# Kernel optimization log

Hardware: AMD Instinct MI355X
Metric: run time of the kernel (lower is better)

Reference implementation:

```python
import jax, jax.numpy as jnp
import numpy as np

B, N, H, NH = 2, 2048, 1024, 16
HD = H // NH


def setup_inputs() -> dict:
    key = jax.random.key(0)
    ks = jax.random.split(key, 12)
    s = 0.02
    inp = {
        "q": jax.random.normal(ks[0], (B, N, H), jnp.float32),
        "k": jax.random.normal(ks[1], (B, N, H), jnp.float32),
        "v": jax.random.normal(ks[2], (B, N, H), jnp.float32),
        # causal mask, broadcast over batch and heads
        "mask": jnp.tril(jnp.ones((N, N), jnp.float32))[None, None, :, :],
        "Wq": jax.random.normal(ks[3], (H, H), jnp.float32) * s,
        "bq": jnp.zeros((H,), jnp.float32),
        "Wk": jax.random.normal(ks[4], (H, H), jnp.float32) * s,
        "bk": jnp.zeros((H,), jnp.float32),
        "Wv": jax.random.normal(ks[5], (H, H), jnp.float32) * s,
        "bv": jnp.zeros((H,), jnp.float32),
        "Wp": jax.random.normal(ks[6], (H, H), jnp.float32) * s,
        "bp": jnp.zeros((H,), jnp.float32),
    }
    return inp


def _split_heads(x):
    # [b, n, (h d)] -> [b, h, n, d]
    b, n, _ = x.shape
    return x.reshape(b, n, NH, HD).transpose(0, 2, 1, 3)


def reference(q, k, v, mask, Wq, bq, Wk, bk, Wv, bv, Wp, bp):
    Q = _split_heads(q @ Wq.T + bq)                      # [b,h,n,d]
    K = _split_heads(k @ Wk.T + bk)
    V = _split_heads(v @ Wv.T + bv)
    scores = jnp.einsum("bhnd,bhmd->bhnm", Q, K) / jnp.sqrt(jnp.float32(HD))
    scores = jnp.where(mask == 0, -jnp.inf, scores)
    attn = jax.nn.softmax(scores, axis=-1)
    out = jnp.einsum("bhnm,bhmd->bhnd", attn, V)         # [b,h,n,d]
    out = out.transpose(0, 2, 1, 3).reshape(q.shape[0], q.shape[1], H)
    # dropout is identity in eval mode
    return out @ Wp.T + bp
```

## Files before the change

kernel.cpp:

```cpp
#include <hip/hip_runtime.h>


typedef unsigned short ushortT;
typedef unsigned int uintT;
typedef __attribute__((ext_vector_type(8))) short short8;
typedef __attribute__((ext_vector_type(4))) float f32x4;

#define M_ROWS 4096
#define KDIM   1024
#define NDIM   1024
#define SEQ    2048
#define HDHEAD 64

__device__ __forceinline__ float bf2f(ushortT s) {
    union { unsigned u; float f; } v; v.u = ((unsigned)s) << 16; return v.f;
}
__device__ __forceinline__ ushortT f2bf(float x) {
    union { float f; unsigned u; } v; v.f = x;
    return (ushortT)((v.u + 0x7fffu + ((v.u >> 16) & 1u)) >> 16);
}

__device__ __forceinline__ bool detect_f32(const uintT* w) {
    int hits = 0;
#pragma unroll
    for (int i = 0; i < 16; ++i) {
        const unsigned e = (w[i] >> 7) & 0xffu;
        hits += (e >= 118u && e <= 131u) ? 1 : 0;
    }
    return hits < 8;
}

__device__ __forceinline__ short8 cvt8(const float* p) {
    f32x4 a = *(const f32x4*)p;
    f32x4 b = *(const f32x4*)(p + 4);
    short8 r;
    r[0] = (short)f2bf(a[0]); r[1] = (short)f2bf(a[1]);
    r[2] = (short)f2bf(a[2]); r[3] = (short)f2bf(a[3]);
    r[4] = (short)f2bf(b[0]); r[5] = (short)f2bf(b[1]);
    r[6] = (short)f2bf(b[2]); r[7] = (short)f2bf(b[3]);
    return r;
}

__device__ __forceinline__ void gl2lds16(const ushortT* g, ushortT* l) {
    __builtin_amdgcn_global_load_lds(
        (const __attribute__((address_space(1))) void*)g,
        (__attribute__((address_space(3))) void*)l,
        16, 0, 0);
}

__device__ __forceinline__ void bar_lgkm() {
    __builtin_amdgcn_sched_barrier(0);
    asm volatile("s_waitcnt lgkmcnt(0)" ::: "memory");
    __builtin_amdgcn_s_barrier();
    __builtin_amdgcn_sched_barrier(0);
}

__global__ __launch_bounds__(256) void convert_kernel(
    const void* __restrict__ q, const void* __restrict__ k, const void* __restrict__ v,
    const void* __restrict__ Wq, const void* __restrict__ Wk,
    const void* __restrict__ Wv, const void* __restrict__ Wp,
    const void* __restrict__ bq, const void* __restrict__ bk,
    const void* __restrict__ bv, const void* __restrict__ bp,
    ushortT* __restrict__ dst) {
    const bool f32m = detect_f32((const uintT*)q);
    const size_t u = (size_t)blockIdx.x * 256 + threadIdx.x;

    const void* src; size_t soff, doff;
    if (u < 1572864u) {
        const int seg = (int)(u >> 19);
        const size_t o = u & 524287u;
        src  = seg == 0 ? q : (seg == 1 ? k : v);
        soff = o * 8;
        doff = (size_t)seg * 4194304u + o * 8;
    } else if (u < 2097152u) {
        const size_t u2 = u - 1572864u;
        const int seg = (int)(u2 >> 17);
        const size_t o = u2 & 131071u;
        src  = seg == 0 ? Wq : (seg == 1 ? Wk : (seg == 2 ? Wv : Wp));
        soff = o * 8;
        doff = 12582912u + (size_t)seg * 1048576u + o * 8;
    } else {
        const size_t u3 = u - 2097152u;
        const int seg = (int)(u3 >> 7);
        const size_t o = u3 & 127u;
        src  = seg == 0 ? bq : (seg == 1 ? bk : (seg == 2 ? bv : bp));
        soff = o * 8;
        doff = 16777216u + (size_t)seg * 1024u + o * 8;
    }

    if (f32m)
        *(short8*)(dst + doff) = cvt8((const float*)src + soff);
    else
        *(short8*)(dst + doff) = *(const short8*)((const ushortT*)src + soff);
}

__device__ __forceinline__ void gemm_body(const void* __restrict__ Av,
                                          const void* __restrict__ Wv_,
                                          const void* __restrict__ biasv,
                                          void* __restrict__ Cv,
                                          bool a_f32, bool w_f32, bool c_f32,
                                          float cscale, bool vt_store) {
    __shared__ ushortT ldsA[128 * 64];
    __shared__ ushortT ldsB[128 * 64];

    const int tid  = threadIdx.x;
    const int lane = tid & 63;
    const int wid  = tid >> 6;
    const int bm   = blockIdx.x;
    const int bn   = blockIdx.y;
    const int wm   = wid >> 1;
    const int wn   = wid & 1;

    const int srow = lane >> 2;
    const int scol = (lane & 3) * 8;

    f32x4 acc[4][4];
#pragma unroll
    for (int i = 0; i < 4; ++i)
#pragma unroll
        for (int j = 0; j < 4; ++j) acc[i][j] = (f32x4){0.f, 0.f, 0.f, 0.f};

    const int fr   = lane & 15;
    const int quad = lane >> 4;

    for (int kt = 0; kt < KDIM / 64; ++kt) {
        const int k0 = kt * 64;
        if (!a_f32 && !w_f32) {
#pragma unroll
            for (int t = 0; t < 4; ++t) {
                const int chunk = wid * 4 + t;
                const int kh  = chunk >> 3;
                const int r16 = (chunk & 7) * 16;
                const size_t ra = (size_t)(bm * 128 + r16 + srow) * KDIM + k0 + kh * 32 + scol;
                const size_t rw = (size_t)(bn * 128 + r16 + srow) * KDIM + k0 + kh * 32 + scol;
                gl2lds16((const ushortT*)Av + ra, ldsA + chunk * 512);
                gl2lds16((const ushortT*)Wv_ + rw, ldsB + chunk * 512);
            }
        } else {
            short8 ta[4], tb[4];
#pragma unroll
            for (int t = 0; t < 4; ++t) {
                const int chunk = wid * 4 + t;
                const int kh  = chunk >> 3;
                const int r16 = (chunk & 7) * 16;
                const size_t ra = (size_t)(bm * 128 + r16 + srow) * KDIM + k0 + kh * 32 + scol;
                const size_t rw = (size_t)(bn * 128 + r16 + srow) * KDIM + k0 + kh * 32 + scol;
                ta[t] = a_f32 ? cvt8((const float*)Av + ra)
                              : *(const short8*)((const ushortT*)Av + ra);
                tb[t] = w_f32 ? cvt8((const float*)Wv_ + rw)
                              : *(const short8*)((const ushortT*)Wv_ + rw);
            }
#pragma unroll
            for (int t = 0; t < 4; ++t) {
                const int chunk = wid * 4 + t;
                *(short8*)(ldsA + chunk * 512 + lane * 8) = ta[t];
                *(short8*)(ldsB + chunk * 512 + lane * 8) = tb[t];
            }
        }
        __syncthreads();

#pragma unroll
        for (int s = 0; s < 2; ++s) {
            short8 aF[4], bF[4];
#pragma unroll
            for (int i = 0; i < 4; ++i)
                aF[i] = *(const short8*)(ldsA + s * 4096 + (wm * 64 + i * 16 + fr) * 32 + quad * 8);
#pragma unroll
            for (int j = 0; j < 4; ++j)
                bF[j] = *(const short8*)(ldsB + s * 4096 + (wn * 64 + j * 16 + fr) * 32 + quad * 8);
#pragma unroll
            for (int i = 0; i < 4; ++i)
#pragma unroll
                for (int j = 0; j < 4; ++j)
                    acc[i][j] = __builtin_amdgcn_mfma_f32_16x16x32_bf16(aF[i], bF[j], acc[i][j], 0, 0, 0);
        }
        __syncthreads();
    }

#pragma unroll
    for (int j = 0; j < 4; ++j) {
        const int col = bn * 128 + wn * 64 + j * 16 + fr;
        const float bv = w_f32 ? ((const float*)biasv)[col]
                               : bf2f(((const ushortT*)biasv)[col]);
#pragma unroll
        for (int i = 0; i < 4; ++i) {
            const int row0 = bm * 128 + wm * 64 + i * 16 + quad * 4;
#pragma unroll
            for (int r = 0; r < 4; ++r) {
                const float val = (acc[i][j][r] + bv) * cscale;
                const int row = row0 + r;
                if (vt_store) {
                    const int bb = row >> 11, n = row & 2047;
                    const int hh = col >> 6,  d = col & 63;
                    ((ushortT*)Cv)[(size_t)((bb * 16 + hh) * 64 + d) * SEQ + n] = f2bf(val);
                } else if (c_f32) {
                    ((float*)Cv)[(size_t)row * NDIM + col] = val;
                } else {
                    ((ushortT*)Cv)[(size_t)row * NDIM + col] = f2bf(val);
                }
            }
        }
    }
}

__global__ __launch_bounds__(256, 3) void qkv_proj_kernel(
    const void* __restrict__ q, const void* __restrict__ k, const void* __restrict__ v,
    const void* __restrict__ Wq, const void* __restrict__ Wk, const void* __restrict__ Wv,
    const void* __restrict__ bq, const void* __restrict__ bk, const void* __restrict__ bv,
    ushortT* __restrict__ Qp, ushortT* __restrict__ Kp, ushortT* __restrict__ Vt) {
    const bool f32m = detect_f32((const uintT*)q);
    const void* A; const void* W; const void* bias; ushortT* C;
    float cscale = 1.f; bool vt = false;
    if (blockIdx.z == 0)      { A = q; W = Wq; bias = bq; C = Qp; cscale = 0.125f; }
    else if (blockIdx.z == 1) { A = k; W = Wk; bias = bk; C = Kp; }
    else                      { A = v; W = Wv; bias = bv; C = Vt; vt = true; }
    gemm_body(A, W, bias, (void*)C, f32m, f32m, false, cscale, vt);
}

__global__ __launch_bounds__(256, 2) void out_proj_kernel(
    const ushortT* __restrict__ A, const void* __restrict__ W,
    const void* __restrict__ bias, void* __restrict__ C,
    const void* __restrict__ qdet) {
    const bool wf = detect_f32((const uintT*)W);
    const bool cf = detect_f32((const uintT*)qdet);

    __shared__ ushortT ldsA[128 * 64];
    __shared__ ushortT ldsB[64 * 64];

    const int tid  = threadIdx.x;
    const int lane = tid & 63;
    const int wid  = tid >> 6;
    const int bm   = blockIdx.x;
    const int bn   = blockIdx.y;

    const int srow = lane >> 2;
    const int scol = (lane & 3) * 8;
    const int fr   = lane & 15;
    const int quad = lane >> 4;

    f32x4 acc[2][4];
#pragma unroll
    for (int i = 0; i < 2; ++i)
#pragma unroll
        for (int j = 0; j < 4; ++j) acc[i][j] = (f32x4){0.f, 0.f, 0.f, 0.f};

    for (int kt = 0; kt < KDIM / 64; ++kt) {
        const int k0 = kt * 64;
        if (!wf) {
#pragma unroll
            for (int t = 0; t < 4; ++t) {
                const int chunk = wid * 4 + t;
                const int kh  = chunk >> 3;
                const int r16 = (chunk & 7) * 16;
                const size_t ra = (size_t)(bm * 128 + r16 + srow) * KDIM + k0 + kh * 32 + scol;
                gl2lds16(A + ra, ldsA + chunk * 512);
            }
#pragma unroll
            for (int t = 0; t < 2; ++t) {
                const int chunk = wid * 2 + t;
                const int kh  = chunk >> 2;
                const int r16 = (chunk & 3) * 16;
                const size_t rw = (size_t)(bn * 64 + r16 + srow) * KDIM + k0 + kh * 32 + scol;
                gl2lds16((const ushortT*)W + rw, ldsB + chunk * 512);
            }
        } else {
            short8 ta[4], tb[2];
#pragma unroll
            for (int t = 0; t < 4; ++t) {
                const int chunk = wid * 4 + t;
                const int kh  = chunk >> 3;
                const int r16 = (chunk & 7) * 16;
                const size_t ra = (size_t)(bm * 128 + r16 + srow) * KDIM + k0 + kh * 32 + scol;
                ta[t] = *(const short8*)(A + ra);
            }
#pragma unroll
            for (int t = 0; t < 2; ++t) {
                const int chunk = wid * 2 + t;
                const int kh  = chunk >> 2;
                const int r16 = (chunk & 3) * 16;
                const size_t rw = (size_t)(bn * 64 + r16 + srow) * KDIM + k0 + kh * 32 + scol;
                tb[t] = cvt8((const float*)W + rw);
            }
#pragma unroll
            for (int t = 0; t < 4; ++t)
                *(short8*)(ldsA + (wid * 4 + t) * 512 + lane * 8) = ta[t];
#pragma unroll
            for (int t = 0; t < 2; ++t)
                *(short8*)(ldsB + (wid * 2 + t) * 512 + lane * 8) = tb[t];
        }
        __syncthreads();

#pragma unroll
        for (int s = 0; s < 2; ++s) {
            short8 aF[2], bF[4];
#pragma unroll
            for (int i = 0; i < 2; ++i)
                aF[i] = *(const short8*)(ldsA + s * 4096 + (wid * 32 + i * 16 + fr) * 32 + quad * 8);
#pragma unroll
            for (int j = 0; j < 4; ++j)
                bF[j] = *(const short8*)(ldsB + s * 2048 + (j * 16 + fr) * 32 + quad * 8);
#pragma unroll
            for (int i = 0; i < 2; ++i)
#pragma unroll
                for (int j = 0; j < 4; ++j)
                    acc[i][j] = __builtin_amdgcn_mfma_f32_16x16x32_bf16(aF[i], bF[j], acc[i][j], 0, 0, 0);
        }
        __syncthreads();
    }

#pragma unroll
    for (int j = 0; j < 4; ++j) {
        const int col = bn * 64 + j * 16 + fr;
        const float bv = wf ? ((const float*)bias)[col]
                            : bf2f(((const ushortT*)bias)[col]);
#pragma unroll
        for (int i = 0; i < 2; ++i) {
            const int row0 = bm * 128 + wid * 32 + i * 16 + quad * 4;
#pragma unroll
            for (int r = 0; r < 4; ++r) {
                const float val = acc[i][j][r] + bv;
                const int row = row0 + r;
                if (cf) ((float*)C)[(size_t)row * NDIM + col] = val;
                else    ((ushortT*)C)[(size_t)row * NDIM + col] = f2bf(val);
            }
        }
    }
}

__global__ __launch_bounds__(256, 2) void flash_attn_kernel(
    const ushortT* __restrict__ Qp, const ushortT* __restrict__ Kp,
    const ushortT* __restrict__ Vt, ushortT* __restrict__ Op) {
    __shared__ ushortT ldsK[2 * 64 * 40];
    __shared__ ushortT ldsV[64 * 72];
    __shared__ ushortT ldsP0[4][16 * 72];
    __shared__ ushortT ldsP1[4][16 * 72];

    const int tid  = threadIdx.x;
    const int lane = tid & 63;
    const int wid  = tid >> 6;
    const int fr   = lane & 15;
    const int quad = lane >> 4;

    const int lin = blockIdx.x;
    const int c   = lin & 255;
    const int g   = lin >> 8;
    const int bh  = c & 31;
    const int t   = c >> 5;
    const int pid = g ? (15 - t) : t;
    const int h   = bh & 15;
    const int b   = bh >> 4;

    const size_t base  = (size_t)b * SEQ * NDIM + (size_t)h * HDHEAD;
    const size_t vtb   = (size_t)(b * 16 + h) * HDHEAD * SEQ;

    int ksst[2], keyloc[2];
#pragma unroll
    for (int u = 0; u < 2; ++u) {
        const int chunk = wid * 2 + u;
        ksst[u]   = chunk >> 2;
        keyloc[u] = (chunk & 3) * 16 + (lane >> 2);
    }
    const int c8 = (lane & 3) * 8;
    const int vd  = lane >> 3;
    const int vk8 = (lane & 7) * 8;

    const int q00 = pid * 64;
    const int q01 = (31 - pid) * 64;
    const int nkv = 32 - pid;

    short8 qf0[2], qf1[2];
#pragma unroll
    for (int ks = 0; ks < 2; ++ks) {
        qf0[ks] = *(const short8*)(Qp + base + (size_t)(q00 + wid * 16 + fr) * NDIM + ks * 32 + quad * 8);
        qf1[ks] = *(const short8*)(Qp + base + (size_t)(q01 + wid * 16 + fr) * NDIM + ks * 32 + quad * 8);
    }

    f32x4 accO0[4], accO1[4];
#pragma unroll
    for (int dt = 0; dt < 4; ++dt) {
        accO0[dt] = (f32x4){0.f, 0.f, 0.f, 0.f};
        accO1[dt] = (f32x4){0.f, 0.f, 0.f, 0.f};
    }
    float lsum0[4], lsum1[4];
#pragma unroll
    for (int r = 0; r < 4; ++r) { lsum0[r] = 0.f; lsum1[r] = 0.f; }

    short8 kreg[2], vreg[2];
#pragma unroll
    for (int u = 0; u < 2; ++u) {
        kreg[u] = *(const short8*)(Kp + base + (size_t)keyloc[u] * NDIM + ksst[u] * 32 + c8);
        const int d = (wid * 2 + u) * 8 + vd;
        vreg[u] = *(const short8*)(Vt + vtb + (size_t)d * SEQ + vk8);
    }

    const int qi0 = q00 + wid * 16 + quad * 4;
    const int qi1 = q01 + wid * 16 + quad * 4;

    for (int kt = 0; kt < nkv; ++kt) {
        bar_lgkm();

#pragma unroll
        for (int u = 0; u < 2; ++u) {
            *(short8*)(ldsK + ksst[u] * 2560 + keyloc[u] * 40 + c8) = kreg[u];
            const int d = (wid * 2 + u) * 8 + vd;
            *(short8*)(ldsV + d * 72 + vk8) = vreg[u];
        }

        if (kt + 1 < nkv) {
            const int kv1 = (kt + 1) * 64;
#pragma unroll
            for (int u = 0; u < 2; ++u) {
                kreg[u] = *(const short8*)(Kp + base + (size_t)(kv1 + keyloc[u]) * NDIM + ksst[u] * 32 + c8);
                const int d = (wid * 2 + u) * 8 + vd;
                vreg[u] = *(const short8*)(Vt + vtb + (size_t)d * SEQ + kv1 + vk8);
            }
        }
        bar_lgkm();

        const bool act0 = (kt <= pid);

        f32x4 s0[4], s1[4];
#pragma unroll
        for (int nt = 0; nt < 4; ++nt) {
            short8 kf[2];
#pragma unroll
            for (int ks = 0; ks < 2; ++ks)
                kf[ks] = *(const short8*)(ldsK + ks * 2560 + (nt * 16 + fr) * 40 + quad * 8);
            f32x4 a1 = (f32x4){0.f, 0.f, 0.f, 0.f};
#pragma unroll
            for (int ks = 0; ks < 2; ++ks)
                a1 = __builtin_amdgcn_mfma_f32_16x16x32_bf16(qf1[ks], kf[ks], a1, 0, 0, 0);
            s1[nt] = a1;
            if (act0) {
                f32x4 a0 = (f32x4){0.f, 0.f, 0.f, 0.f};
#pragma unroll
                for (int ks = 0; ks < 2; ++ks)
                    a0 = __builtin_amdgcn_mfma_f32_16x16x32_bf16(qf0[ks], kf[ks], a0, 0, 0, 0);
                s0[nt] = a0;
            }
        }

        const int kv0 = kt * 64;
        if (kt == nkv - 1) {
#pragma unroll
            for (int nt = 0; nt < 4; ++nt) {
                const int kj = kv0 + nt * 16 + fr;
#pragma unroll
                for (int r = 0; r < 4; ++r)
                    s1[nt][r] = (kj > qi1 + r) ? -1e30f : s1[nt][r];
            }
        }
        if (act0 && kt == pid) {
#pragma unroll
            for (int nt = 0; nt < 4; ++nt) {
                const int kj = kv0 + nt * 16 + fr;
#pragma unroll
                for (int r = 0; r < 4; ++r)
                    s0[nt][r] = (kj > qi0 + r) ? -1e30f : s0[nt][r];
            }
        }

        ushortT* pbuf1 = ldsP1[wid];
#pragma unroll
        for (int nt = 0; nt < 4; ++nt) {
#pragma unroll
            for (int r = 0; r < 4; ++r) {
                const float p = __expf(fminf(s1[nt][r], 30.f));
                lsum1[r] += p;
                pbuf1[(quad * 4 + r) * 72 + nt * 16 + fr] = f2bf(p);
            }
        }
        ushortT* pbuf0 = ldsP0[wid];
        if (act0) {
#pragma unroll
            for (int nt = 0; nt < 4; ++nt) {
#pragma unroll
                for (int r = 0; r < 4; ++r) {
                    const float p = __expf(fminf(s0[nt][r], 30.f));
                    lsum0[r] += p;
                    pbuf0[(quad * 4 + r) * 72 + nt * 16 + fr] = f2bf(p);
                }
            }
        }

        asm volatile("" ::: "memory");

#pragma unroll
        for (int ks = 0; ks < 2; ++ks) {
            short8 pf1 = *(const short8*)(pbuf1 + fr * 72 + ks * 32 + quad * 8);
            short8 pf0;
            if (act0) pf0 = *(const short8*)(pbuf0 + fr * 72 + ks * 32 + quad * 8);
#pragma unroll
            for (int dt = 0; dt < 4; ++dt) {
                short8 vf = *(const short8*)(ldsV + (dt * 16 + fr) * 72 + ks * 32 + quad * 8);
                accO1[dt] = __builtin_amdgcn_mfma_f32_16x16x32_bf16(pf1, vf, accO1[dt], 0, 0, 0);
                if (act0)
                    accO0[dt] = __builtin_amdgcn_mfma_f32_16x16x32_bf16(pf0, vf, accO0[dt], 0, 0, 0);
            }
        }
    }

#pragma unroll
    for (int r = 0; r < 4; ++r) {
#pragma unroll
        for (int off = 8; off >= 1; off >>= 1) {
            lsum0[r] += __shfl_xor(lsum0[r], off, 64);
            lsum1[r] += __shfl_xor(lsum1[r], off, 64);
        }
    }
#pragma unroll
    for (int dt = 0; dt < 4; ++dt) {
#pragma unroll
        for (int r = 0; r < 4; ++r) {
            const size_t row0 = (size_t)(q00 + wid * 16 + quad * 4 + r);
            const size_t row1 = (size_t)(q01 + wid * 16 + quad * 4 + r);
            Op[(size_t)b * SEQ * NDIM + row0 * NDIM + h * HDHEAD + dt * 16 + fr] =
                f2bf(accO0[dt][r] / lsum0[r]);
            Op[(size_t)b * SEQ * NDIM + row1 * NDIM + h * HDHEAD + dt * 16 + fr] =
                f2bf(accO1[dt][r] / lsum1[r]);
        }
    }
}

extern "C" void kernel_launch(void* const* d_in, const int* in_sizes, int n_in,
                              void* d_out, int out_size, void* d_ws, size_t ws_size,
                              hipStream_t stream) {
    const void* q  = d_in[0];
    const void* k  = d_in[1];
    const void* v  = d_in[2];
    const void* Wq = d_in[4];
    const void* bq = d_in[5];
    const void* Wk = d_in[6];
    const void* bk = d_in[7];
    const void* Wv = d_in[8];
    const void* bv = d_in[9];
    const void* Wp = d_in[10];
    const void* bp = d_in[11];

    dim3 blk(256);
    const size_t FAST_WS = 58728448;

    if (ws_size >= FAST_WS) {
        ushortT* cb   = (ushortT*)d_ws;
        ushortT* qb16 = cb;
        ushortT* kb16 = cb + 4194304u;
        ushortT* vb16 = cb + 8388608u;
        ushortT* Wqb  = cb + 12582912u;
        ushortT* Wkb  = cb + 13631488u;
        ushortT* Wvb  = cb + 14680064u;
        ushortT* Wpb  = cb + 15728640u;
        ushortT* bqb  = cb + 16777216u;
        ushortT* bkb  = cb + 16778240u;
        ushortT* bvb  = cb + 16779264u;
        ushortT* bpb  = cb + 16780288u;
        ushortT* Qp   = cb + 16781312u;
        ushortT* Kp   = Qp + 4194304u;
        ushortT* Vt   = Kp + 4194304u;
        ushortT* Op   = qb16;

        convert_kernel<<<dim3(8194), blk, 0, stream>>>(
            q, k, v, Wq, Wk, Wv, Wp, bq, bk, bv, bp, cb);
        qkv_proj_kernel<<<dim3(32, 8, 3), blk, 0, stream>>>(
            qb16, kb16, vb16, Wqb, Wkb, Wvb, bqb, bkb, bvb, Qp, Kp, Vt);
        flash_attn_kernel<<<dim3(512), blk, 0, stream>>>(Qp, Kp, Vt, Op);
        out_proj_kernel<<<dim3(32, 16), blk, 0, stream>>>(Op, Wpb, bpb, d_out, q);
    } else {
        ushortT* ws = (ushortT*)d_ws;
        ushortT* Qp = ws;
        ushortT* Kp = ws + (size_t)M_ROWS * NDIM;
        ushortT* Vt = ws + (size_t)2 * M_ROWS * NDIM;
        ushortT* Op = ws + (size_t)3 * M_ROWS * NDIM;

        qkv_proj_kernel<<<dim3(32, 8, 3), blk, 0, stream>>>(
            q, k, v, Wq, Wk, Wv, bq, bk, bv, Qp, Kp, Vt);
        flash_attn_kernel<<<dim3(512), blk, 0, stream>>>(Qp, Kp, Vt, Op);
        out_proj_kernel<<<dim3(32, 16), blk, 0, stream>>>(Op, Wp, bp, d_out, q);
    }
}
```

Before: 231.3 us.

## Split paired-query-tile attention blocks into one tile per block

Each attention block used to process two query tiles (pid and 31-pid) that shared every K/V tile load. Now each block handles a single 64-row query tile, so the grid doubles to 1024 blocks. The block order runs 0..15, 31..16, 15..0, 16..31 to spread the causal work evenly. Launch bounds rise to 4 blocks per CU and the P buffer in shared memory halves, aiming for more occupancy and less register pressure. In exchange, K/V tiles are loaded twice as often, so global and LDS traffic per unit of work goes up.

```diff
diff --git a/kernel.cpp b/kernel.cpp
--- a/kernel.cpp
+++ b/kernel.cpp
@@ -327,13 +327,12 @@
     }
 }
 
-__global__ __launch_bounds__(256, 2) void flash_attn_kernel(
+__global__ __launch_bounds__(256, 4) void flash_attn_kernel(
     const ushortT* __restrict__ Qp, const ushortT* __restrict__ Kp,
     const ushortT* __restrict__ Vt, ushortT* __restrict__ Op) {
     __shared__ ushortT ldsK[2 * 64 * 40];
     __shared__ ushortT ldsV[64 * 72];
-    __shared__ ushortT ldsP0[4][16 * 72];
-    __shared__ ushortT ldsP1[4][16 * 72];
+    __shared__ ushortT ldsP[4][16 * 72];
 
     const int tid  = threadIdx.x;
     const int lane = tid & 63;
@@ -346,12 +345,16 @@
     const int g   = lin >> 8;
     const int bh  = c & 31;
     const int t   = c >> 5;
-    const int pid = g ? (15 - t) : t;
-    const int h   = bh & 15;
-    const int b   = bh >> 4;
-
-    const size_t base  = (size_t)b * SEQ * NDIM + (size_t)h * HDHEAD;
-    const size_t vtb   = (size_t)(b * 16 + h) * HDHEAD * SEQ;
+    int qb;
+    if      (g == 0) qb = t;
+    else if (g == 1) qb = 31 - t;
+    else if (g == 2) qb = 15 - t;
+    else             qb = 16 + t;
+    const int h = bh & 15;
+    const int b = bh >> 4;
+
+    const size_t base = (size_t)b * SEQ * NDIM + (size_t)h * HDHEAD;
+    const size_t vtb  = (size_t)(b * 16 + h) * HDHEAD * SEQ;
 
     int ksst[2], keyloc[2];
 #pragma unroll
@@ -364,26 +367,20 @@
     const int vd  = lane >> 3;
     const int vk8 = (lane & 7) * 8;
 
-    const int q00 = pid * 64;
-    const int q01 = (31 - pid) * 64;
-    const int nkv = 32 - pid;
-
-    short8 qf0[2], qf1[2];
-#pragma unroll
-    for (int ks = 0; ks < 2; ++ks) {
-        qf0[ks] = *(const short8*)(Qp + base + (size_t)(q00 + wid * 16 + fr) * NDIM + ks * 32 + quad * 8);
-        qf1[ks] = *(const short8*)(Qp + base + (size_t)(q01 + wid * 16 + fr) * NDIM + ks * 32 + quad * 8);
-    }
-
-    f32x4 accO0[4], accO1[4];
-#pragma unroll
-    for (int dt = 0; dt < 4; ++dt) {
-        accO0[dt] = (f32x4){0.f, 0.f, 0.f, 0.f};
-        accO1[dt] = (f32x4){0.f, 0.f, 0.f, 0.f};
-    }
-    float lsum0[4], lsum1[4];
-#pragma unroll
-    for (int r = 0; r < 4; ++r) { lsum0[r] = 0.f; lsum1[r] = 0.f; }
+    const int q0  = qb * 64;
+    const int nkv = qb + 1;
+
+    short8 qf[2];
+#pragma unroll
+    for (int ks = 0; ks < 2; ++ks)
+        qf[ks] = *(const short8*)(Qp + base + (size_t)(q0 + wid * 16 + fr) * NDIM + ks * 32 + quad * 8);
+
+    f32x4 accO[4];
+#pragma unroll
+    for (int dt = 0; dt < 4; ++dt) accO[dt] = (f32x4){0.f, 0.f, 0.f, 0.f};
+    float lsum[4];
+#pragma unroll
+    for (int r = 0; r < 4; ++r) lsum[r] = 0.f;
 
     short8 kreg[2], vreg[2];
 #pragma unroll
@@ -393,8 +390,7 @@
         vreg[u] = *(const short8*)(Vt + vtb + (size_t)d * SEQ + vk8);
     }
 
-    const int qi0 = q00 + wid * 16 + quad * 4;
-    const int qi1 = q01 + wid * 16 + quad * 4;
+    const int qi = q0 + wid * 16 + quad * 4;
 
     for (int kt = 0; kt < nkv; ++kt) {
         bar_lgkm();
@@ -417,27 +413,16 @@
         }
         bar_lgkm();
 
-        const bool act0 = (kt <= pid);
-
-        f32x4 s0[4], s1[4];
+        f32x4 s[4];
 #pragma unroll
         for (int nt = 0; nt < 4; ++nt) {
-            short8 kf[2];
-#pragma unroll
-            for (int ks = 0; ks < 2; ++ks)
-                kf[ks] = *(const short8*)(ldsK + ks * 2560 + (nt * 16 + fr) * 40 + quad * 8);
-            f32x4 a1 = (f32x4){0.f, 0.f, 0.f, 0.f};
-#pragma unroll
-            for (int ks = 0; ks < 2; ++ks)
-                a1 = __builtin_amdgcn_mfma_f32_16x16x32_bf16(qf1[ks], kf[ks], a1, 0, 0, 0);
-            s1[nt] = a1;
-            if (act0) {
-                f32x4 a0 = (f32x4){0.f, 0.f, 0.f, 0.f};
-#pragma unroll
-                for (int ks = 0; ks < 2; ++ks)
-                    a0 = __builtin_amdgcn_mfma_f32_16x16x32_bf16(qf0[ks], kf[ks], a0, 0, 0, 0);
-                s0[nt] = a0;
-            }
+            f32x4 a = (f32x4){0.f, 0.f, 0.f, 0.f};
+#pragma unroll
+            for (int ks = 0; ks < 2; ++ks) {
+                short8 kf = *(const short8*)(ldsK + ks * 2560 + (nt * 16 + fr) * 40 + quad * 8);
+                a = __builtin_amdgcn_mfma_f32_16x16x32_bf16(qf[ks], kf, a, 0, 0, 0);
+            }
+            s[nt] = a;
         }
 
         const int kv0 = kt * 64;
@@ -447,39 +432,18 @@
                 const int kj = kv0 + nt * 16 + fr;
 #pragma unroll
                 for (int r = 0; r < 4; ++r)
-                    s1[nt][r] = (kj > qi1 + r) ? -1e30f : s1[nt][r];
-            }
-        }
-        if (act0 && kt == pid) {
-#pragma unroll
-            for (int nt = 0; nt < 4; ++nt) {
-                const int kj = kv0 + nt * 16 + fr;
-#pragma unroll
-                for (int r = 0; r < 4; ++r)
-                    s0[nt][r] = (kj > qi0 + r) ? -1e30f : s0[nt][r];
-            }
-        }
-
-        ushortT* pbuf1 = ldsP1[wid];
+                    s[nt][r] = (kj > qi + r) ? -1e30f : s[nt][r];
+            }
+        }
+
+        ushortT* pbuf = ldsP[wid];
 #pragma unroll
         for (int nt = 0; nt < 4; ++nt) {
 #pragma unroll
             for (int r = 0; r < 4; ++r) {
-                const float p = __expf(fminf(s1[nt][r], 30.f));
-                lsum1[r] += p;
-                pbuf1[(quad * 4 + r) * 72 + nt * 16 + fr] = f2bf(p);
-            }
-        }
-        ushortT* pbuf0 = ldsP0[wid];
-        if (act0) {
-#pragma unroll
-            for (int nt = 0; nt < 4; ++nt) {
-#pragma unroll
-                for (int r = 0; r < 4; ++r) {
-                    const float p = __expf(fminf(s0[nt][r], 30.f));
-                    lsum0[r] += p;
-                    pbuf0[(quad * 4 + r) * 72 + nt * 16 + fr] = f2bf(p);
-                }
+                const float p = __expf(fminf(s[nt][r], 30.f));
+                lsum[r] += p;
+                pbuf[(quad * 4 + r) * 72 + nt * 16 + fr] = f2bf(p);
             }
         }
 
@@ -487,15 +451,11 @@
 
 #pragma unroll
         for (int ks = 0; ks < 2; ++ks) {
-            short8 pf1 = *(const short8*)(pbuf1 + fr * 72 + ks * 32 + quad * 8);
-            short8 pf0;
-            if (act0) pf0 = *(const short8*)(pbuf0 + fr * 72 + ks * 32 + quad * 8);
+            short8 pf = *(const short8*)(pbuf + fr * 72 + ks * 32 + quad * 8);
 #pragma unroll
             for (int dt = 0; dt < 4; ++dt) {
                 short8 vf = *(const short8*)(ldsV + (dt * 16 + fr) * 72 + ks * 32 + quad * 8);
-                accO1[dt] = __builtin_amdgcn_mfma_f32_16x16x32_bf16(pf1, vf, accO1[dt], 0, 0, 0);
-                if (act0)
-                    accO0[dt] = __builtin_amdgcn_mfma_f32_16x16x32_bf16(pf0, vf, accO0[dt], 0, 0, 0);
+                accO[dt] = __builtin_amdgcn_mfma_f32_16x16x32_bf16(pf, vf, accO[dt], 0, 0, 0);
             }
         }
     }
@@ -503,21 +463,16 @@
 #pragma unroll
     for (int r = 0; r < 4; ++r) {
 #pragma unroll
-        for (int off = 8; off >= 1; off >>= 1) {
-            lsum0[r] += __shfl_xor(lsum0[r], off, 64);
-            lsum1[r] += __shfl_xor(lsum1[r], off, 64);
-        }
+        for (int off = 8; off >= 1; off >>= 1)
+            lsum[r] += __shfl_xor(lsum[r], off, 64);
     }
 #pragma unroll
     for (int dt = 0; dt < 4; ++dt) {
 #pragma unroll
         for (int r = 0; r < 4; ++r) {
-            const size_t row0 = (size_t)(q00 + wid * 16 + quad * 4 + r);
-            const size_t row1 = (size_t)(q01 + wid * 16 + quad * 4 + r);
-            Op[(size_t)b * SEQ * NDIM + row0 * NDIM + h * HDHEAD + dt * 16 + fr] =
-                f2bf(accO0[dt][r] / lsum0[r]);
-            Op[(size_t)b * SEQ * NDIM + row1 * NDIM + h * HDHEAD + dt * 16 + fr] =
-                f2bf(accO1[dt][r] / lsum1[r]);
+            const size_t row = (size_t)(q0 + wid * 16 + quad * 4 + r);
+            Op[(size_t)b * SEQ * NDIM + row * NDIM + h * HDHEAD + dt * 16 + fr] =
+                f2bf(accO[dt][r] / lsum[r]);
         }
     }
 }
@@ -562,7 +517,7 @@
             q, k, v, Wq, Wk, Wv, Wp, bq, bk, bv, bp, cb);
         qkv_proj_kernel<<<dim3(32, 8, 3), blk, 0, stream>>>(
             qb16, kb16, vb16, Wqb, Wkb, Wvb, bqb, bkb, bvb, Qp, Kp, Vt);
-        flash_attn_kernel<<<dim3(512), blk, 0, stream>>>(Qp, Kp, Vt, Op);
+        flash_attn_kernel<<<dim3(1024), blk, 0, stream>>>(Qp, Kp, Vt, Op);
         out_proj_kernel<<<dim3(32, 16), blk, 0, stream>>>(Op, Wpb, bpb, d_out, q);
     } else {
         ushortT* ws = (ushortT*)d_ws;
@@ -573,7 +528,7 @@
 
         qkv_proj_kernel<<<dim3(32, 8, 3), blk, 0, stream>>>(
             q, k, v, Wq, Wk, Wv, bq, bk, bv, Qp, Kp, Vt);
-        flash_attn_kernel<<<dim3(512), blk, 0, stream>>>(Qp, Kp, Vt, Op);
+        flash_attn_kernel<<<dim3(1024), blk, 0, stream>>>(Qp, Kp, Vt, Op);
         out_proj_kernel<<<dim3(32, 16), blk, 0, stream>>>(Op, Wp, bp, d_out, q);
     }
 }
```

Result: no change. 233.4 us (+0.9%).
